# Kernel optimization log

Hardware: AMD Instinct MI355X
Metric: run time of the kernel (lower is better)

The kernel has to match this reference:

```python
import jax, jax.numpy as jnp
import numpy as np

NUM_EXPERTS = 8
TOP_K = 2

def setup_inputs() -> dict:
    key = jax.random.key(0)
    ks = jax.random.split(key, 7)
    T, D, H, E = 4096, 1024, 4096, NUM_EXPERTS
    s_in = (2.0 / (D + H)) ** 0.5   # xavier-ish scale for W1
    s_out = (2.0 / (H + D)) ** 0.5
    return {
        "x": jax.random.normal(ks[0], (T, D), jnp.float32),
        "Wg": jax.random.normal(ks[1], (D, E), jnp.float32) * 0.02,
        "bg": jnp.zeros((E,), jnp.float32),
        "W1": jax.random.normal(ks[2], (E, D, H), jnp.float32) * s_in,
        "b1": jnp.zeros((E, H), jnp.float32),
        "W2": jax.random.normal(ks[3], (E, H, D), jnp.float32) * s_out,
        "b2": jnp.zeros((E, D), jnp.float32),
    }

def reference(x, Wg, bg, W1, b1, W2, b2):
    # x: [T, D]; gate over E experts
    gate = jax.nn.softmax(x @ Wg + bg, axis=-1)            # [T, E]
    _, top_idx = jax.lax.top_k(gate, TOP_K)                # [T, K]
    # mask[t, e] = True iff expert e is among top-k for token t
    mask = jnp.any(top_idx[:, :, None] == jnp.arange(NUM_EXPERTS)[None, None, :], axis=1)
    combine_w = jnp.where(mask, gate, 0.0)                 # [T, E]
    # out = sum_e combine_w[:, e] * MLP_e(x); non-selected tokens get weight 0
    out = jnp.zeros_like(x)
    for e in range(NUM_EXPERTS):  # small fixed expert loop
        h = jax.nn.relu(x @ W1[e] + b1[e])                 # [T, H]
        y = h @ W2[e] + b2[e]                              # [T, D]
        out = out + combine_w[:, e:e + 1] * y
    return out
```

## Files before the change

kernel.cpp:

```cpp
#include <hip/hip_runtime.h>
#include <stdint.h>

#define T_TOK 4096
#define DDIM  1024
#define HDIM  4096
#define NEXP  8
#define MAXTILES 72

typedef short s16x8  __attribute__((ext_vector_type(8)));
typedef short s16x4  __attribute__((ext_vector_type(4)));
typedef float f32x4t __attribute__((ext_vector_type(4)));

#define GLOAD16(gp, lp) __builtin_amdgcn_global_load_lds( \
    (const __attribute__((address_space(1))) unsigned int*)(gp), \
    (__attribute__((address_space(3))) unsigned int*)(lp), 16, 0, 0)

__device__ __forceinline__ unsigned short f2b(float f){
  unsigned int u = __float_as_uint(f);
  u += 0x7fffu + ((u >> 16) & 1u);
  return (unsigned short)(u >> 16);
}

__global__ void gate_kernel(const float* __restrict__ x, const float* __restrict__ Wg,
                            const float* __restrict__ bg,
                            int* __restrict__ topk_e, float* __restrict__ topk_w){
  const int t = blockIdx.x;
  const int lane = threadIdx.x;
  const float* xr = x + (size_t)t * DDIM;
  float acc[NEXP];
  #pragma unroll
  for (int e = 0; e < NEXP; ++e) acc[e] = 0.f;
  #pragma unroll 4
  for (int it = 0; it < DDIM/64; ++it){
    int i = it*64 + lane;
    float xi = xr[i];
    const float4* wr = (const float4*)(Wg + (size_t)i * NEXP);
    float4 w0 = wr[0], w1 = wr[1];
    acc[0] += xi*w0.x; acc[1] += xi*w0.y; acc[2] += xi*w0.z; acc[3] += xi*w0.w;
    acc[4] += xi*w1.x; acc[5] += xi*w1.y; acc[6] += xi*w1.z; acc[7] += xi*w1.w;
  }
  #pragma unroll
  for (int e = 0; e < NEXP; ++e){
    float v = acc[e];
    #pragma unroll
    for (int off = 32; off > 0; off >>= 1) v += __shfl_xor(v, off, 64);
    acc[e] = v;
  }
  if (lane == 0){
    float l[NEXP], m = -1e30f;
    #pragma unroll
    for (int e = 0; e < NEXP; ++e){ l[e] = acc[e] + bg[e]; m = fmaxf(m, l[e]); }
    float p[NEXP], s = 0.f;
    #pragma unroll
    for (int e = 0; e < NEXP; ++e){ p[e] = expf(l[e] - m); s += p[e]; }
    float inv = 1.f / s;
    int a1 = 0; float v1 = -1.f;
    #pragma unroll
    for (int e = 0; e < NEXP; ++e){ p[e] *= inv; if (p[e] > v1){ v1 = p[e]; a1 = e; } }
    int a2 = -1; float v2 = -1.f;
    #pragma unroll
    for (int e = 0; e < NEXP; ++e){ if (e == a1) continue; if (p[e] > v2){ v2 = p[e]; a2 = e; } }
    topk_e[2*t]   = a1; topk_w[2*t]   = v1;
    topk_e[2*t+1] = a2; topk_w[2*t+1] = v2;
  }
}

__global__ void route_count(const int* __restrict__ topk_e, const float* __restrict__ topk_w,
                            int* __restrict__ expertList, float* __restrict__ pairW,
                            int* __restrict__ counts){
  const int e = blockIdx.x;
  const int tid = threadIdx.x;
  __shared__ int pfx[256];
  __shared__ int base_s;
  if (tid == 0) base_s = 0;
  __syncthreads();
  for (int c = 0; c < T_TOK/256; ++c){
    int t = c*256 + tid;
    int e0 = topk_e[2*t], e1 = topk_e[2*t+1];
    int sel = 0; float w = 0.f;
    if (e0 == e){ sel = 1; w = topk_w[2*t]; }
    else if (e1 == e){ sel = 1; w = topk_w[2*t+1]; }
    pfx[tid] = sel;
    __syncthreads();
    for (int off = 1; off < 256; off <<= 1){
      int v = (tid >= off) ? pfx[tid - off] : 0;
      __syncthreads();
      pfx[tid] += v;
      __syncthreads();
    }
    if (sel){
      int pos = base_s + pfx[tid] - 1;
      expertList[e*T_TOK + pos] = t;
      pairW[e*T_TOK + pos] = w;
    }
    __syncthreads();
    if (tid == 0) base_s += pfx[255];
    __syncthreads();
  }
  if (tid == 0) counts[e] = base_s;
}

__global__ void plan_kernel(const int* __restrict__ counts, int* __restrict__ nTiles,
                            int* __restrict__ tileExpert, int* __restrict__ tileStart){
  if (blockIdx.x != 0 || threadIdx.x != 0) return;
  int nt = 0;
  for (int e = 0; e < NEXP; ++e){
    int c = counts[e];
    int tcount = (c + 127) >> 7;
    for (int i = 0; i < tcount; ++i){ tileExpert[nt] = e; tileStart[nt] = i*128; ++nt; }
  }
  *nTiles = nt;
}

__global__ void conv_x(const float* __restrict__ x, unsigned short* __restrict__ xb){
  int i = (blockIdx.x*256 + threadIdx.x)*4;
  float4 v = *(const float4*)(x + i);
  s16x4 o;
  o[0] = (short)f2b(v.x); o[1] = (short)f2b(v.y);
  o[2] = (short)f2b(v.z); o[3] = (short)f2b(v.w);
  *(s16x4*)(xb + i) = o;
}

__global__ __launch_bounds__(256)
void transpose_w(const float* __restrict__ W, unsigned short* __restrict__ Wt,
                 int K, int N){
  const int e = blockIdx.z;
  const float* Wb = W + (size_t)e*K*N;
  unsigned short* Wtb = Wt + (size_t)e*K*N;
  const int n0 = blockIdx.x*64, k0 = blockIdx.y*64;
  __shared__ unsigned short t[64][72];
  const int r  = threadIdx.x >> 4;
  const int c4 = (threadIdx.x & 15) * 4;
  #pragma unroll
  for (int i = 0; i < 4; ++i){
    int k = r + i*16;
    float4 v = *(const float4*)(Wb + (size_t)(k0+k)*N + n0 + c4);
    t[c4+0][k] = f2b(v.x); t[c4+1][k] = f2b(v.y);
    t[c4+2][k] = f2b(v.z); t[c4+3][k] = f2b(v.w);
  }
  __syncthreads();
  const int kk = (threadIdx.x & 7) * 8;
  #pragma unroll
  for (int i = 0; i < 2; ++i){
    int n = (threadIdx.x >> 3) + i*32;
    s16x8 v;
    #pragma unroll
    for (int j = 0; j < 8; ++j) v[j] = (short)t[n][kk+j];
    *(s16x8*)(Wtb + (size_t)(n0+n)*K + k0 + kk) = v;
  }
}

template<int LAYER>
__global__ __launch_bounds__(256)
void moe_gemm(const unsigned short* __restrict__ Abf,
              const unsigned short* __restrict__ Wt,
              const float* __restrict__ bias,
              const int* __restrict__ nTilesPtr,
              const int* __restrict__ tileExpert,
              const int* __restrict__ tileStart,
              const int* __restrict__ counts,
              const int* __restrict__ expertList,
              const float* __restrict__ pairW,
              unsigned short* __restrict__ Hout,
              float* __restrict__ out)
{
  const int tile = blockIdx.x;
  if (tile >= *nTilesPtr) return;
  constexpr int KD = (LAYER == 1) ? DDIM : HDIM;
  constexpr int ND = (LAYER == 1) ? HDIM : DDIM;
  const int e   = tileExpert[tile];
  const int ts  = tileStart[tile];
  const int cnt = counts[e];
  const int n0  = blockIdx.y * 128;
  const int tid  = threadIdx.x;
  const int lane = tid & 63;
  const int wave = tid >> 6;
  const int wm = (wave >> 1) * 64;
  const int wn = (wave & 1) * 64;

  __shared__ __align__(16) unsigned short As[128][64];
  __shared__ __align__(16) unsigned short Bs[128][64];
  __shared__ int   tokenBuf[128];
  __shared__ float wBuf[128];

  if (tid < 128){
    int pos = ts + tid;
    int tok = 0; float w = 0.f;
    if (pos < cnt){ tok = expertList[e*T_TOK + pos]; w = pairW[e*T_TOK + pos]; }
    tokenBuf[tid] = tok; wBuf[tid] = w;
  }
  __syncthreads();

  const int rsub = tid >> 3;
  const int koff = (tid & 7) * 8;
  const unsigned short* gA[4];
  const unsigned short* gB[4];
  #pragma unroll
  for (int g = 0; g < 4; ++g){
    const int row = g*32 + rsub;
    if (LAYER == 1) gA[g] = Abf + (size_t)tokenBuf[row]*DDIM + koff;
    else            gA[g] = Abf + (size_t)(tile*128 + row)*HDIM + koff;
    gB[g] = Wt + ((size_t)e*ND + n0 + row)*KD + koff;
  }
  unsigned short* ldsA = &As[0][0] + wave*512;
  unsigned short* ldsB = &Bs[0][0] + wave*512;

  f32x4t acc[4][4] = {};
  const int fr = lane & 15;
  const int fq = lane >> 4;

  for (int ko = 0; ko < KD; ko += 64){
    #pragma unroll
    for (int g = 0; g < 4; ++g){
      GLOAD16(gA[g] + ko, ldsA + g*2048);
      GLOAD16(gB[g] + ko, ldsB + g*2048);
    }
    __syncthreads();
    #pragma unroll
    for (int ks = 0; ks < 2; ++ks){
      s16x8 af[4], bf[4];
      #pragma unroll
      for (int mf = 0; mf < 4; ++mf) af[mf] = *(const s16x8*)&As[wm + mf*16 + fr][ks*32 + fq*8];
      #pragma unroll
      for (int nf = 0; nf < 4; ++nf) bf[nf] = *(const s16x8*)&Bs[wn + nf*16 + fr][ks*32 + fq*8];
      #pragma unroll
      for (int mf = 0; mf < 4; ++mf)
        #pragma unroll
        for (int nf = 0; nf < 4; ++nf)
          acc[mf][nf] = __builtin_amdgcn_mfma_f32_16x16x32_bf16(af[mf], bf[nf], acc[mf][nf], 0, 0, 0);
    }
    __syncthreads();
  }

  const int rb = wm + fq*4;
  const int cb = wn + fr;
  if (LAYER == 1){
    #pragma unroll
    for (int mf = 0; mf < 4; ++mf){
      #pragma unroll
      for (int nf = 0; nf < 4; ++nf){
        int c = cb + nf*16;
        float b = bias[e*HDIM + n0 + c];
        #pragma unroll
        for (int j = 0; j < 4; ++j){
          int r = rb + mf*16 + j;
          float v = fmaxf(acc[mf][nf][j] + b, 0.f);
          Hout[(size_t)(tile*128 + r)*HDIM + n0 + c] = f2b(v);
        }
      }
    }
  } else {
    #pragma unroll
    for (int mf = 0; mf < 4; ++mf){
      #pragma unroll
      for (int j = 0; j < 4; ++j){
        int r = rb + mf*16 + j;
        if (ts + r < cnt){
          int tok = tokenBuf[r];
          float w = wBuf[r];
          #pragma unroll
          for (int nf = 0; nf < 4; ++nf){
            int c = cb + nf*16;
            float v = w * (acc[mf][nf][j] + bias[e*DDIM + n0 + c]);
            atomicAdd(out + (size_t)tok*DDIM + n0 + c, v);
          }
        }
      }
    }
  }
}

extern "C" void kernel_launch(void* const* d_in, const int* in_sizes, int n_in,
                              void* d_out, int out_size, void* d_ws, size_t ws_size,
                              hipStream_t stream){
  const float* x  = (const float*)d_in[0];
  const float* Wg = (const float*)d_in[1];
  const float* bg = (const float*)d_in[2];
  const float* W1 = (const float*)d_in[3];
  const float* b1 = (const float*)d_in[4];
  const float* W2 = (const float*)d_in[5];
  const float* b2 = (const float*)d_in[6];
  float* out = (float*)d_out;

  char* p = (char*)d_ws;
  int*   topk_e     = (int*)p;   p += (size_t)T_TOK*2*sizeof(int);
  float* topk_w     = (float*)p; p += (size_t)T_TOK*2*sizeof(float);
  int*   counts     = (int*)p;   p += 8*sizeof(int);
  int*   nTiles     = (int*)p;   p += 8*sizeof(int);
  int*   tileExpert = (int*)p;   p += 128*sizeof(int);
  int*   tileStart  = (int*)p;   p += 128*sizeof(int);
  int*   expertList = (int*)p;   p += (size_t)NEXP*T_TOK*sizeof(int);
  float* pairW      = (float*)p; p += (size_t)NEXP*T_TOK*sizeof(float);
  p = (char*)(((uintptr_t)p + 255) & ~(uintptr_t)255);
  unsigned short* xb = (unsigned short*)p;
  p += (size_t)T_TOK*DDIM*sizeof(unsigned short);
  p = (char*)(((uintptr_t)p + 255) & ~(uintptr_t)255);
  unsigned short* Wtbuf = (unsigned short*)p;
  p += (size_t)NEXP*DDIM*HDIM*sizeof(unsigned short);
  p = (char*)(((uintptr_t)p + 255) & ~(uintptr_t)255);
  unsigned short* Hact = (unsigned short*)p;

  hipMemsetAsync(d_out, 0, (size_t)T_TOK*DDIM*sizeof(float), stream);
  gate_kernel<<<T_TOK, 64, 0, stream>>>(x, Wg, bg, topk_e, topk_w);
  route_count<<<NEXP, 256, 0, stream>>>(topk_e, topk_w, expertList, pairW, counts);
  plan_kernel<<<1, 1, 0, stream>>>(counts, nTiles, tileExpert, tileStart);
  conv_x<<<T_TOK*DDIM/1024, 256, 0, stream>>>(x, xb);

  transpose_w<<<dim3(HDIM/64, DDIM/64, NEXP), 256, 0, stream>>>(W1, Wtbuf, DDIM, HDIM);
  moe_gemm<1><<<dim3(MAXTILES, HDIM/128), 256, 0, stream>>>(
      xb, Wtbuf, b1, nTiles, tileExpert, tileStart, counts, expertList, pairW, Hact, nullptr);

  transpose_w<<<dim3(DDIM/64, HDIM/64, NEXP), 256, 0, stream>>>(W2, Wtbuf, HDIM, DDIM);
  moe_gemm<2><<<dim3(MAXTILES, DDIM/128), 256, 0, stream>>>(
      Hact, Wtbuf, b2, nTiles, tileExpert, tileStart, counts, expertList, pairW, nullptr, out);
}
```

Baseline: 464.3 us.

## Double-buffer LDS tiles in MoE GEMM and remap blocks per XCD

New measurement: 548.7 us. 18.2% more time.

```diff
diff --git a/kernel.cpp b/kernel.cpp
--- a/kernel.cpp
+++ b/kernel.cpp
@@ -164,22 +164,30 @@
               unsigned short* __restrict__ Hout,
               float* __restrict__ out)
 {
-  const int tile = blockIdx.x;
-  if (tile >= *nTilesPtr) return;
   constexpr int KD = (LAYER == 1) ? DDIM : HDIM;
   constexpr int ND = (LAYER == 1) ? HDIM : DDIM;
+  constexpr int NT = KD / 64;
+
+  const int nwg = gridDim.x;
+  const int b   = blockIdx.x;
+  const int q = nwg >> 3, r = nwg & 7;
+  const int xcd = b & 7, ii = b >> 3;
+  const int lin = (xcd < r ? xcd*(q+1) : r*(q+1) + (xcd-r)*q) + ii;
+  const int tile = lin % MAXTILES;
+  const int n0   = (lin / MAXTILES) * 128;
+
+  if (tile >= *nTilesPtr) return;
   const int e   = tileExpert[tile];
   const int ts  = tileStart[tile];
   const int cnt = counts[e];
-  const int n0  = blockIdx.y * 128;
   const int tid  = threadIdx.x;
   const int lane = tid & 63;
   const int wave = tid >> 6;
   const int wm = (wave >> 1) * 64;
   const int wn = (wave & 1) * 64;
 
-  __shared__ __align__(16) unsigned short As[128][64];
-  __shared__ __align__(16) unsigned short Bs[128][64];
+  __shared__ __align__(16) unsigned short As[2][128][64];
+  __shared__ __align__(16) unsigned short Bs[2][128][64];
   __shared__ int   tokenBuf[128];
   __shared__ float wBuf[128];
 
@@ -202,27 +210,33 @@
     else            gA[g] = Abf + (size_t)(tile*128 + row)*HDIM + koff;
     gB[g] = Wt + ((size_t)e*ND + n0 + row)*KD + koff;
   }
-  unsigned short* ldsA = &As[0][0] + wave*512;
-  unsigned short* ldsB = &Bs[0][0] + wave*512;
+
+  auto STAGE = [&](int buf, int ko){
+    unsigned short* la = &As[buf][0][0] + wave*512;
+    unsigned short* lb = &Bs[buf][0][0] + wave*512;
+    #pragma unroll
+    for (int g = 0; g < 4; ++g){
+      GLOAD16(gA[g] + ko, la + g*2048);
+      GLOAD16(gB[g] + ko, lb + g*2048);
+    }
+  };
 
   f32x4t acc[4][4] = {};
   const int fr = lane & 15;
   const int fq = lane >> 4;
 
-  for (int ko = 0; ko < KD; ko += 64){
-    #pragma unroll
-    for (int g = 0; g < 4; ++g){
-      GLOAD16(gA[g] + ko, ldsA + g*2048);
-      GLOAD16(gB[g] + ko, ldsB + g*2048);
-    }
-    __syncthreads();
+  STAGE(0, 0);
+  __syncthreads();
+  int cur = 0;
+  for (int t = 0; t < NT; ++t){
+    if (t < NT-1) STAGE(cur ^ 1, (t+1)*64);
     #pragma unroll
     for (int ks = 0; ks < 2; ++ks){
       s16x8 af[4], bf[4];
       #pragma unroll
-      for (int mf = 0; mf < 4; ++mf) af[mf] = *(const s16x8*)&As[wm + mf*16 + fr][ks*32 + fq*8];
-      #pragma unroll
-      for (int nf = 0; nf < 4; ++nf) bf[nf] = *(const s16x8*)&Bs[wn + nf*16 + fr][ks*32 + fq*8];
+      for (int mf = 0; mf < 4; ++mf) af[mf] = *(const s16x8*)&As[cur][wm + mf*16 + fr][ks*32 + fq*8];
+      #pragma unroll
+      for (int nf = 0; nf < 4; ++nf) bf[nf] = *(const s16x8*)&Bs[cur][wn + nf*16 + fr][ks*32 + fq*8];
       #pragma unroll
       for (int mf = 0; mf < 4; ++mf)
         #pragma unroll
@@ -230,6 +244,7 @@
           acc[mf][nf] = __builtin_amdgcn_mfma_f32_16x16x32_bf16(af[mf], bf[nf], acc[mf][nf], 0, 0, 0);
     }
     __syncthreads();
+    cur ^= 1;
   }
 
   const int rb = wm + fq*4;
@@ -240,12 +255,12 @@
       #pragma unroll
       for (int nf = 0; nf < 4; ++nf){
         int c = cb + nf*16;
-        float b = bias[e*HDIM + n0 + c];
+        float bsv = bias[e*HDIM + n0 + c];
         #pragma unroll
         for (int j = 0; j < 4; ++j){
-          int r = rb + mf*16 + j;
-          float v = fmaxf(acc[mf][nf][j] + b, 0.f);
-          Hout[(size_t)(tile*128 + r)*HDIM + n0 + c] = f2b(v);
+          int rr = rb + mf*16 + j;
+          float v = fmaxf(acc[mf][nf][j] + bsv, 0.f);
+          Hout[(size_t)(tile*128 + rr)*HDIM + n0 + c] = f2b(v);
         }
       }
     }
@@ -254,10 +269,10 @@
     for (int mf = 0; mf < 4; ++mf){
       #pragma unroll
       for (int j = 0; j < 4; ++j){
-        int r = rb + mf*16 + j;
-        if (ts + r < cnt){
-          int tok = tokenBuf[r];
-          float w = wBuf[r];
+        int rr = rb + mf*16 + j;
+        if (ts + rr < cnt){
+          int tok = tokenBuf[rr];
+          float w = wBuf[rr];
           #pragma unroll
           for (int nf = 0; nf < 4; ++nf){
             int c = cb + nf*16;
@@ -307,10 +322,10 @@
   conv_x<<<T_TOK*DDIM/1024, 256, 0, stream>>>(x, xb);
 
   transpose_w<<<dim3(HDIM/64, DDIM/64, NEXP), 256, 0, stream>>>(W1, Wtbuf, DDIM, HDIM);
-  moe_gemm<1><<<dim3(MAXTILES, HDIM/128), 256, 0, stream>>>(
+  moe_gemm<1><<<MAXTILES*(HDIM/128), 256, 0, stream>>>(
       xb, Wtbuf, b1, nTiles, tileExpert, tileStart, counts, expertList, pairW, Hact, nullptr);
 
   transpose_w<<<dim3(DDIM/64, HDIM/64, NEXP), 256, 0, stream>>>(W2, Wtbuf, HDIM, DDIM);
-  moe_gemm<2><<<dim3(MAXTILES, DDIM/128), 256, 0, stream>>>(
+  moe_gemm<2><<<MAXTILES*(DDIM/128), 256, 0, stream>>>(
       Hact, Wtbuf, b2, nTiles, tileExpert, tileStart, counts, expertList, pairW, nullptr, out);
 }
```
